# Kernel tuning notes

Measured on AMD Instinct MI355X. Metric: run time of the kernel, lower is better.

The kernel has to match this reference:

```python
import math
import jax, jax.numpy as jnp
from jax import lax
import numpy as np

B, T, DIM = 2, 1024, 512
EXPAND, D_STATE, CONV_K, NUM_SCALES = 2, 16, 4, 3
D_INNER = EXPAND * DIM
DT_RANK = D_INNER // 16


def parallel_scan_log(log_coeffs, log_values):
    # h_t = a_t*h_{t-1} + b_t via Heinsen log-space scan
    a_star = jnp.cumsum(log_coeffs, axis=1)
    return jnp.exp(a_star + lax.cumlogsumexp(log_values - a_star, axis=1))


def selective_scan(x, dt, A, B_ssm, C_ssm, D_p):
    Bb, Tt, di = x.shape
    ds = A.shape[1]
    dt = jax.nn.softplus(dt)
    dA = jnp.exp(dt[..., None] * A[None, None])                    # (B,T,di,ds)
    dBx = dt[..., None] * B_ssm[:, :, None, :] * x[..., None]      # (B,T,di,ds)
    log_dA = jnp.log(jnp.maximum(dA, 1e-38)).reshape(Bb, Tt, di * ds)
    log_dBx = jnp.log(jnp.maximum(dBx, 1e-38)).reshape(Bb, Tt, di * ds)
    h = parallel_scan_log(log_dA, log_dBx).reshape(Bb, Tt, di, ds)
    return jnp.einsum('bts,btds->btd', C_ssm, h) + D_p * x


def ssm_core(x, conv_w, conv_b, xproj_w, dtproj_w, dtproj_b, A_log, D_p):
    di = x.shape[-1]
    # depthwise causal conv1d: left-pad K-1 (== torch pad K-1 both sides + truncate to T)
    xc = lax.conv_general_dilated(x.transpose(0, 2, 1), conv_w, (1,), [(CONV_K - 1, 0)],
                                  dimension_numbers=('NCH', 'OIH', 'NCH'),
                                  feature_group_count=di)
    xc = jax.nn.silu((xc + conv_b[None, :, None]).transpose(0, 2, 1))
    proj = xc @ xproj_w.T
    dt_raw = proj[..., :DT_RANK]
    B_ssm = proj[..., DT_RANK:DT_RANK + D_STATE]
    C_ssm = proj[..., DT_RANK + D_STATE:]
    dt = dt_raw @ dtproj_w.T + dtproj_b
    A = -jnp.exp(A_log)
    return selective_scan(xc, dt, A, B_ssm, C_ssm, D_p)


def downsample(x, stride):
    if stride == 1:
        return x
    Bb, Tt, Dd = x.shape
    Tt2 = Tt // stride * stride
    return x[:, :Tt2].reshape(Bb, Tt2 // stride, stride, Dd).mean(axis=2)


def upsample(x, T_target):
    Bb, T_src, Dd = x.shape
    if T_src == T_target:
        return x
    factor = math.ceil(T_target / T_src)
    x_up = jnp.repeat(x, factor, axis=1)[:, :T_target]
    if x_up.shape[1] < T_target:
        pad = jnp.broadcast_to(x_up[:, -1:], (Bb, T_target - x_up.shape[1], Dd))
        x_up = jnp.concatenate([x_up, pad], axis=1)
    return x_up


def forward(x, in_proj_w, conv_w, conv_b, xproj_w, dtproj_w, dtproj_b, A_log, D_p,
            scale_weights, cg_w1, cg_w2, out_proj_w, ln_gamma, ln_beta):
    Tt = x.shape[1]
    residual = x
    xz = x @ in_proj_w.T
    x_in, gate = xz[..., :D_INNER], xz[..., D_INNER:]
    outs = []
    for s in range(NUM_SCALES):
        x_s = downsample(x_in, 2 ** s)
        y_s = ssm_core(x_s, conv_w[s], conv_b[s], xproj_w[s], dtproj_w[s],
                       dtproj_b[s], A_log[s], D_p[s])
        outs.append(upsample(y_s, Tt))
    w = jax.nn.softmax(scale_weights)
    fused = sum(w[s] * outs[s] for s in range(NUM_SCALES))
    ctx = jnp.mean(jnp.stack(outs, axis=0), axis=0)
    cg = jax.nn.sigmoid(jax.nn.silu(ctx @ cg_w1.T) @ cg_w2.T)
    fused = fused * cg
    out = (fused * jax.nn.silu(gate)) @ out_proj_w.T
    y = out + residual
    mu = jnp.mean(y, axis=-1, keepdims=True)
    var = jnp.var(y, axis=-1, keepdims=True)
    return (y - mu) / jnp.sqrt(var + 1e-5) * ln_gamma + ln_beta


def setup_inputs():
    key = jax.random.key(0)
    ks = jax.random.split(key, 12)
    x = jax.random.normal(ks[0], (B, T, DIM), jnp.float32)
    in_proj_w = jax.random.normal(ks[1], (2 * D_INNER, DIM), jnp.float32) * (1.0 / math.sqrt(DIM))
    conv_w = jax.random.normal(ks[2], (NUM_SCALES, D_INNER, 1, CONV_K), jnp.float32) * 0.3
    conv_b = jax.random.normal(ks[3], (NUM_SCALES, D_INNER), jnp.float32) * 0.05
    xproj_w = jax.random.normal(ks[4], (NUM_SCALES, DT_RANK + 2 * D_STATE, D_INNER), jnp.float32) * 0.02
    dtproj_w = jax.random.normal(ks[5], (NUM_SCALES, D_INNER, DT_RANK), jnp.float32) * 0.05
    dtproj_b = jax.random.uniform(ks[6], (NUM_SCALES, D_INNER), jnp.float32,
                                  math.log(0.001), math.log(0.1))
    A_log = jnp.broadcast_to(jnp.log(jnp.arange(1, D_STATE + 1, dtype=jnp.float32)),
                             (NUM_SCALES, D_INNER, D_STATE))
    D_p = jnp.ones((NUM_SCALES, D_INNER), jnp.float32)
    scale_weights = jnp.ones((NUM_SCALES,), jnp.float32)
    cg_w1 = jax.random.normal(ks[7], (D_INNER // 2, D_INNER), jnp.float32) * (1.0 / math.sqrt(D_INNER))
    cg_w2 = jax.random.normal(ks[8], (D_INNER, D_INNER // 2), jnp.float32) * (1.0 / math.sqrt(D_INNER // 2))
    out_proj_w = jax.random.normal(ks[9], (DIM, D_INNER), jnp.float32) * (1.0 / math.sqrt(D_INNER))
    ln_gamma = jnp.ones((DIM,), jnp.float32)
    ln_beta = jnp.zeros((DIM,), jnp.float32)
    return {"x": x, "in_proj_w": in_proj_w, "conv_w": conv_w, "conv_b": conv_b,
            "xproj_w": xproj_w, "dtproj_w": dtproj_w, "dtproj_b": dtproj_b,
            "A_log": A_log, "D_p": D_p, "scale_weights": scale_weights,
            "cg_w1": cg_w1, "cg_w2": cg_w2, "out_proj_w": out_proj_w,
            "ln_gamma": ln_gamma, "ln_beta": ln_beta}


def reference(x, in_proj_w, conv_w, conv_b, xproj_w, dtproj_w, dtproj_b, A_log, D_p,
              scale_weights, cg_w1, cg_w2, out_proj_w, ln_gamma, ln_beta):
    return forward(x, in_proj_w, conv_w, conv_b, xproj_w, dtproj_w, dtproj_b, A_log,
                   D_p, scale_weights, cg_w1, cg_w2, out_proj_w, ln_gamma, ln_beta)
```

## Files before the change

### kernel.cpp

```cpp
#include <hip/hip_runtime.h>
#include <hip/hip_bf16.h>

#define BATCH   2
#define SEQ     1024
#define DIMSZ   512
#define DINNER  1024
#define DTRANK  64
#define DSTATE  16
#define CHUNK   32

typedef __hip_bfloat16 bf16;
typedef __attribute__((ext_vector_type(8))) short s8v;
typedef __attribute__((ext_vector_type(4))) float f4v;

constexpr size_t OXH    = 0;
constexpr size_t OXL    = 1048576;
constexpr size_t OIPWH  = 2097152;
constexpr size_t OIPWL  = 3145728;
constexpr size_t OXWH   = 4194304;
constexpr size_t OXWL   = 4489216;
constexpr size_t ODTWH  = 4784128;
constexpr size_t ODTWL  = 4980736;
constexpr size_t OCG1H  = 5177344;
constexpr size_t OCG1L  = 5701632;
constexpr size_t OCG2H  = 6225920;
constexpr size_t OCG2L  = 6750208;
constexpr size_t OOPWH  = 7274496;
constexpr size_t OOPWL  = 7798784;
constexpr size_t OPJDTH = 8323072;
constexpr size_t OPJDTL = 8552448;
constexpr size_t OH1H   = 8781824;
constexpr size_t OH1L   = 9830400;
constexpr size_t OFGH   = 10878976;
constexpr size_t OFGL   = 12976128;

__device__ __forceinline__ float sigmoidf_(float x) { return 1.f / (1.f + __expf(-x)); }
__device__ __forceinline__ float siluf_(float x) { return x * sigmoidf_(x); }
__device__ __forceinline__ void split2(float v, bf16& hi, bf16& lo) {
    hi = __float2bfloat16(v);
    lo = __float2bfloat16(v - __bfloat162float(hi));
}
__device__ __forceinline__ void split_store4(const float4 v,
                                             bf16* __restrict__ ph,
                                             bf16* __restrict__ pl) {
    union { bf16 b[4]; uint2 u; } H, L;
    split2(v.x, H.b[0], L.b[0]); split2(v.y, H.b[1], L.b[1]);
    split2(v.z, H.b[2], L.b[2]); split2(v.w, H.b[3], L.b[3]);
    *reinterpret_cast<uint2*>(ph) = H.u;
    *reinterpret_cast<uint2*>(pl) = L.u;
}

__global__ void split_inputs_kernel(
    const float* __restrict__ x,   const float* __restrict__ ipw,
    const float* __restrict__ xw,  const float* __restrict__ dtw,
    const float* __restrict__ c1,  const float* __restrict__ c2,
    const float* __restrict__ opw, bf16* __restrict__ bws)
{
    int blk = blockIdx.x;
    const float* src; size_t off, sz;
    if (blk < 1024)      { src = x;   off = OXH;   sz = 1048576; }
    else if (blk < 2048) { src = ipw; off = OIPWH; sz = 1048576; blk -= 1024; }
    else if (blk < 2336) { src = xw;  off = OXWH;  sz = 294912;  blk -= 2048; }
    else if (blk < 2528) { src = dtw; off = ODTWH; sz = 196608;  blk -= 2336; }
    else if (blk < 3040) { src = c1;  off = OCG1H; sz = 524288;  blk -= 2528; }
    else if (blk < 3552) { src = c2;  off = OCG2H; sz = 524288;  blk -= 3040; }
    else                 { src = opw; off = OOPWH; sz = 524288;  blk -= 3552; }
    int i = blk * 1024 + threadIdx.x * 4;
    float4 v = *reinterpret_cast<const float4*>(src + i);
    split_store4(v, bws + off + i, bws + off + sz + i);
}

template <int ACT, bool ADD_RES, bool DT_MODE, bool CTX_A, bool GATE3, bool OUT_SPLIT>
__global__ __launch_bounds__(256) void mgemm_kernel(
    const bf16* __restrict__ Agh, const bf16* __restrict__ Agl, int lda, int K,
    const bf16* __restrict__ Bgh, const bf16* __restrict__ Bgl,
    const float* __restrict__ bias,
    const float* __restrict__ res,
    const float* __restrict__ gxz,
    const float* __restrict__ yy0,
    const float* __restrict__ yy1,
    const float* __restrict__ yy2,
    const float* __restrict__ swp,
    float* __restrict__ C, bf16* __restrict__ Ch, bf16* __restrict__ Cl, int N)
{
    __shared__ bf16 Ah[64][72], Al[64][72], Bh[64][72], Bl[64][72];

    const int m0 = blockIdx.x * 64;
    const int n0 = blockIdx.y * 64;
    const int tid = threadIdx.x;
    const int wave = tid >> 6;
    const int lane = tid & 63;
    const int wm = (wave >> 1) * 32;
    const int wn = (wave & 1) * 32;
    const int m16 = lane & 15;
    const int q   = lane >> 4;

    int scale = 0;
    if (DT_MODE) scale = (m0 < 2048) ? 0 : ((m0 < 3072) ? 1 : 2);
    const bf16* Bhp = DT_MODE ? (Bgh + (size_t)scale * 1024 * K) : Bgh;
    const bf16* Blp = DT_MODE ? (Bgl + (size_t)scale * 1024 * K) : Bgl;
    const float* bias_p = (ACT == 3) ? (DT_MODE ? bias + (size_t)scale * N : bias) : nullptr;

    f4v acc[2][2];
#pragma unroll
    for (int i = 0; i < 2; i++)
#pragma unroll
        for (int j = 0; j < 2; j++)
#pragma unroll
            for (int r = 0; r < 4; r++) acc[i][j][r] = 0.f;

    const int cch = tid & 15;
    const int c4  = cch * 4;
    const int r0  = tid >> 4;

    const float* a0p[4]; const float* a1p[4]; const float* a2p[4];
    const bf16*  ahp[4]; const bf16*  alp[4];
#pragma unroll
    for (int p = 0; p < 4; p++) {
        int m = m0 + r0 + p * 16;
        if (CTX_A) {
            int b = m >> 10, t = m & 1023;
            a0p[p] = yy0 + (size_t)m * 1024 + c4;
            a1p[p] = yy1 + (size_t)((b << 9) + (t >> 1)) * 1024 + c4;
            a2p[p] = yy2 + (size_t)((b << 8) + (t >> 2)) * 1024 + c4;
        } else {
            ahp[p] = Agh + (size_t)m * lda + c4;
            alp[p] = Agl + (size_t)m * lda + c4;
        }
    }
    const bf16* Bh_b = Bhp + (size_t)(n0 + r0) * K + c4;
    const bf16* Bl_b = Blp + (size_t)(n0 + r0) * K + c4;

    const int nkt = K >> 6;
    float4 raf[4]; uint2 rah[4], ral[4], rbh[4], rbl[4];
#pragma unroll
    for (int p = 0; p < 4; p++) {
        if (CTX_A) {
            float4 u = *reinterpret_cast<const float4*>(a0p[p]);
            float4 v = *reinterpret_cast<const float4*>(a1p[p]);
            float4 w = *reinterpret_cast<const float4*>(a2p[p]);
            raf[p] = make_float4((u.x + v.x + w.x) * (1.f / 3.f), (u.y + v.y + w.y) * (1.f / 3.f),
                                 (u.z + v.z + w.z) * (1.f / 3.f), (u.w + v.w + w.w) * (1.f / 3.f));
        } else {
            rah[p] = *reinterpret_cast<const uint2*>(ahp[p]);
            ral[p] = *reinterpret_cast<const uint2*>(alp[p]);
        }
        rbh[p] = *reinterpret_cast<const uint2*>(Bh_b + (size_t)(p * 16) * K);
        rbl[p] = *reinterpret_cast<const uint2*>(Bl_b + (size_t)(p * 16) * K);
    }

    for (int kt = 0; kt < nkt; kt++) {
        if (kt) __syncthreads();
#pragma unroll
        for (int p = 0; p < 4; p++) {
            int r = r0 + p * 16;
            if (CTX_A) {
                split_store4(raf[p], &Ah[r][c4], &Al[r][c4]);
            } else {
                *reinterpret_cast<uint2*>(&Ah[r][c4]) = rah[p];
                *reinterpret_cast<uint2*>(&Al[r][c4]) = ral[p];
            }
            *reinterpret_cast<uint2*>(&Bh[r][c4]) = rbh[p];
            *reinterpret_cast<uint2*>(&Bl[r][c4]) = rbl[p];
        }
        __syncthreads();
        if (kt + 1 < nkt) {
            int off = (kt + 1) * 64;
#pragma unroll
            for (int p = 0; p < 4; p++) {
                if (CTX_A) {
                    float4 u = *reinterpret_cast<const float4*>(a0p[p] + off);
                    float4 v = *reinterpret_cast<const float4*>(a1p[p] + off);
                    float4 w = *reinterpret_cast<const float4*>(a2p[p] + off);
                    raf[p] = make_float4((u.x + v.x + w.x) * (1.f / 3.f), (u.y + v.y + w.y) * (1.f / 3.f),
                                         (u.z + v.z + w.z) * (1.f / 3.f), (u.w + v.w + w.w) * (1.f / 3.f));
                } else {
                    rah[p] = *reinterpret_cast<const uint2*>(ahp[p] + off);
                    ral[p] = *reinterpret_cast<const uint2*>(alp[p] + off);
                }
                rbh[p] = *reinterpret_cast<const uint2*>(Bh_b + off + (size_t)(p * 16) * K);
                rbl[p] = *reinterpret_cast<const uint2*>(Bl_b + off + (size_t)(p * 16) * K);
            }
        }
#pragma unroll
        for (int kk = 0; kk < 2; kk++) {
            const int col = kk * 32 + q * 8;
            s8v ah[2], al[2], bh[2], bl[2];
#pragma unroll
            for (int i = 0; i < 2; i++) {
                int ar = wm + i * 16 + m16;
                ah[i] = *reinterpret_cast<const s8v*>(&Ah[ar][col]);
                al[i] = *reinterpret_cast<const s8v*>(&Al[ar][col]);
                int br = wn + i * 16 + m16;
                bh[i] = *reinterpret_cast<const s8v*>(&Bh[br][col]);
                bl[i] = *reinterpret_cast<const s8v*>(&Bl[br][col]);
            }
#pragma unroll
            for (int i = 0; i < 2; i++)
#pragma unroll
                for (int j = 0; j < 2; j++) {
                    acc[i][j] = __builtin_amdgcn_mfma_f32_16x16x32_bf16(ah[i], bh[j], acc[i][j], 0, 0, 0);
                    acc[i][j] = __builtin_amdgcn_mfma_f32_16x16x32_bf16(al[i], bh[j], acc[i][j], 0, 0, 0);
                    acc[i][j] = __builtin_amdgcn_mfma_f32_16x16x32_bf16(ah[i], bl[j], acc[i][j], 0, 0, 0);
                }
        }
    }

    float e0 = 0.f, e1 = 0.f, e2 = 0.f, inv = 0.f;
    if (GATE3) {
        float s0 = swp[0], s1 = swp[1], s2 = swp[2];
        float mx = fmaxf(s0, fmaxf(s1, s2));
        e0 = __expf(s0 - mx); e1 = __expf(s1 - mx); e2 = __expf(s2 - mx);
        inv = 1.f / (e0 + e1 + e2);
    }

#pragma unroll
    for (int i = 0; i < 2; i++) {
#pragma unroll
        for (int j = 0; j < 2; j++) {
#pragma unroll
            for (int r = 0; r < 4; r++) {
                int gm = m0 + wm + i * 16 + q * 4 + r;
                int gn = n0 + wn + j * 16 + m16;
                float v = acc[i][j][r];
                if (ACT == 3) { v += bias_p[gn]; v = (v > 20.f) ? v : __logf(1.f + __expf(v)); }
                else if (ACT == 1) v = siluf_(v);
                else if (ACT == 2) v = sigmoidf_(v);
                if (GATE3) {
                    int b = gm >> 10, t = gm & 1023;
                    float f = (e0 * yy0[(size_t)gm * 1024 + gn]
                             + e1 * yy1[(size_t)((b << 9) + (t >> 1)) * 1024 + gn]
                             + e2 * yy2[(size_t)((b << 8) + (t >> 2)) * 1024 + gn]) * inv;
                    v = f * v * siluf_(gxz[(size_t)gm * 2048 + 1024 + gn]);
                } else if (ADD_RES) {
                    v += res[(size_t)gm * N + gn];
                }
                if (OUT_SPLIT) {
                    bf16 hh, ll; split2(v, hh, ll);
                    Ch[(size_t)gm * N + gn] = hh;
                    Cl[(size_t)gm * N + gn] = ll;
                } else {
                    C[(size_t)gm * N + gn] = v;
                }
            }
        }
    }
}

__global__ __launch_bounds__(256) void xproj_mfma_kernel(
    const float* __restrict__ A,
    const bf16* __restrict__ xwh, const bf16* __restrict__ xwl,
    float* __restrict__ pj, bf16* __restrict__ pjdth, bf16* __restrict__ pjdtl)
{
    const int K = 1024;
    __shared__ bf16 Ah[64][72], Al[64][72], Bh[64][72], Bl[64][72];

    const int m0 = blockIdx.x * 64;
    const int n0 = blockIdx.y * 64;
    const int tid = threadIdx.x;
    const int wave = tid >> 6;
    const int lane = tid & 63;
    const int wm = (wave >> 1) * 32;
    const int wn = (wave & 1) * 32;
    const int m16 = lane & 15;
    const int q   = lane >> 4;

    const int scale = (m0 < 2048) ? 0 : ((m0 < 3072) ? 1 : 2);
    const bf16* Bhp = xwh + (size_t)scale * 96 * K;
    const bf16* Blp = xwl + (size_t)scale * 96 * K;

    f4v acc[2][2];
#pragma unroll
    for (int i = 0; i < 2; i++)
#pragma unroll
        for (int j = 0; j < 2; j++)
#pragma unroll
            for (int r = 0; r < 4; r++) acc[i][j][r] = 0.f;

    const int cch = tid & 15;
    const int c4  = cch * 4;
    const int r0  = tid >> 4;

    const float* Abase = A + (size_t)(m0 + r0) * K + c4;
    const bf16* Bh_b = Bhp + (size_t)(n0 + r0) * K + c4;
    const bf16* Bl_b = Blp + (size_t)(n0 + r0) * K + c4;
    bool bok[4];
#pragma unroll
    for (int p = 0; p < 4; p++) bok[p] = (n0 + r0 + p * 16) < 96;

    const int nkt = K >> 6;
    float4 ra[4]; uint2 rbh[4], rbl[4];
    const uint2 zero2 = make_uint2(0u, 0u);
#pragma unroll
    for (int p = 0; p < 4; p++) {
        ra[p] = *reinterpret_cast<const float4*>(Abase + (size_t)(p * 16) * K);
        rbh[p] = bok[p] ? *reinterpret_cast<const uint2*>(Bh_b + (size_t)(p * 16) * K) : zero2;
        rbl[p] = bok[p] ? *reinterpret_cast<const uint2*>(Bl_b + (size_t)(p * 16) * K) : zero2;
    }

    for (int kt = 0; kt < nkt; kt++) {
        if (kt) __syncthreads();
#pragma unroll
        for (int p = 0; p < 4; p++) {
            int r = r0 + p * 16;
            split_store4(ra[p], &Ah[r][c4], &Al[r][c4]);
            *reinterpret_cast<uint2*>(&Bh[r][c4]) = rbh[p];
            *reinterpret_cast<uint2*>(&Bl[r][c4]) = rbl[p];
        }
        __syncthreads();
        if (kt + 1 < nkt) {
            int off = (kt + 1) * 64;
#pragma unroll
            for (int p = 0; p < 4; p++) {
                ra[p] = *reinterpret_cast<const float4*>(Abase + off + (size_t)(p * 16) * K);
                rbh[p] = bok[p] ? *reinterpret_cast<const uint2*>(Bh_b + off + (size_t)(p * 16) * K) : zero2;
                rbl[p] = bok[p] ? *reinterpret_cast<const uint2*>(Bl_b + off + (size_t)(p * 16) * K) : zero2;
            }
        }
#pragma unroll
        for (int kk = 0; kk < 2; kk++) {
            const int col = kk * 32 + q * 8;
            s8v ah[2], al[2], bh[2], bl[2];
#pragma unroll
            for (int i = 0; i < 2; i++) {
                int ar = wm + i * 16 + m16;
                ah[i] = *reinterpret_cast<const s8v*>(&Ah[ar][col]);
                al[i] = *reinterpret_cast<const s8v*>(&Al[ar][col]);
                int br = wn + i * 16 + m16;
                bh[i] = *reinterpret_cast<const s8v*>(&Bh[br][col]);
                bl[i] = *reinterpret_cast<const s8v*>(&Bl[br][col]);
            }
#pragma unroll
            for (int i = 0; i < 2; i++)
#pragma unroll
                for (int j = 0; j < 2; j++) {
                    acc[i][j] = __builtin_amdgcn_mfma_f32_16x16x32_bf16(ah[i], bh[j], acc[i][j], 0, 0, 0);
                    acc[i][j] = __builtin_amdgcn_mfma_f32_16x16x32_bf16(al[i], bh[j], acc[i][j], 0, 0, 0);
                    acc[i][j] = __builtin_amdgcn_mfma_f32_16x16x32_bf16(ah[i], bl[j], acc[i][j], 0, 0, 0);
                }
        }
    }

#pragma unroll
    for (int i = 0; i < 2; i++) {
#pragma unroll
        for (int j = 0; j < 2; j++) {
            int gn = n0 + wn + j * 16 + m16;
            if (gn >= 96) continue;
#pragma unroll
            for (int r = 0; r < 4; r++) {
                int gm = m0 + wm + i * 16 + q * 4 + r;
                float v = acc[i][j][r];
                pj[(size_t)gm * 96 + gn] = v;
                if (gn < 64) {
                    bf16 hh, ll; split2(v, hh, ll);
                    pjdth[(size_t)gm * 64 + gn] = hh;
                    pjdtl[(size_t)gm * 64 + gn] = ll;
                }
            }
        }
    }
}

__global__ void conv_fused_kernel(const float* __restrict__ xz,
                                  const float* __restrict__ cw,
                                  const float* __restrict__ cb,
                                  float* __restrict__ xc)
{
    int idx = blockIdx.x * blockDim.x + threadIdx.x;
    if (idx >= 3670016) return;
    int s, rel;
    if (idx < 2097152)      { s = 0; rel = idx; }
    else if (idx < 3145728) { s = 1; rel = idx - 2097152; }
    else                    { s = 2; rel = idx - 3145728; }
    int c = rel & 1023;
    int row = rel >> 10;
    int Ts = 1024 >> s;
    int b = row / Ts;
    int t = row - b * Ts;
    const float* base = xz + (size_t)(b * 1024) * 2048 + c;

    float acc = cb[s * 1024 + c];
#pragma unroll
    for (int k = 0; k < 4; k++) {
        int tau = t - 3 + k;
        if (tau < 0) continue;
        float xv;
        if (s == 0) {
            xv = base[(size_t)tau * 2048];
        } else if (s == 1) {
            xv = 0.5f * (base[(size_t)(2 * tau) * 2048] + base[(size_t)(2 * tau + 1) * 2048]);
        } else {
            xv = 0.25f * (base[(size_t)(4 * tau) * 2048] + base[(size_t)(4 * tau + 1) * 2048]
                        + base[(size_t)(4 * tau + 2) * 2048] + base[(size_t)(4 * tau + 3) * 2048]);
        }
        acc = fmaf(cw[(s * 1024 + c) * 4 + k], xv, acc);
    }
    xc[idx] = siluf_(acc);
}

__device__ __forceinline__ void scan_decode(int blk, int& s, int& nchunk, int& Ts,
                                            int& dquad, int& chunk, int& b, size_t& soff)
{
    int local;
    if (blk < 256)      { s = 0; local = blk;       soff = 0; }
    else if (blk < 384) { s = 1; local = blk - 256; soff = 1048576; }
    else                { s = 2; local = blk - 384; soff = 1572864; }
    nchunk = 32 >> s;
    Ts = 1024 >> s;
    dquad = local & 3;
    chunk = (local >> 2) & (nchunk - 1);
    b = local >> (7 - s);
}

__global__ __launch_bounds__(256) void scan_pass1(
    const float* __restrict__ dt0, const float* __restrict__ xc0, const float* __restrict__ pj0,
    const float* __restrict__ dt1, const float* __restrict__ xc1, const float* __restrict__ pj1,
    const float* __restrict__ dt2, const float* __restrict__ xc2, const float* __restrict__ pj2,
    const float* __restrict__ A_log,
    float* __restrict__ prodA_buf, float* __restrict__ h_buf)
{
    const int jhalf = (blockIdx.x >= 448) ? 1 : 0;
    const int jo = jhalf * 8;
    int s, nchunk, Ts, dquad, chunk, b; size_t soff;
    scan_decode(blockIdx.x - jhalf * 448, s, nchunk, Ts, dquad, chunk, b, soff);
    const float* dt = (s == 0) ? dt0 : (s == 1) ? dt1 : dt2;
    const float* xc = (s == 0) ? xc0 : (s == 1) ? xc1 : xc2;
    const float* pj = (s == 0) ? pj0 : (s == 1) ? pj1 : pj2;

    const int d = dquad * 256 + threadIdx.x;
    const size_t rowbase = (size_t)b * Ts;
    const int t0 = chunk * CHUNK;

    float Acoef[8], h[8], p[8];
#pragma unroll
    for (int j = 0; j < 8; j++) {
        Acoef[j] = -__expf(A_log[((size_t)(s * DINNER + d)) * 16 + jo + j]);
        h[j] = 0.f; p[j] = 1.f;
    }

    __shared__ float bcB[CHUNK][8];
    if (threadIdx.x < CHUNK * 8) {
        int i = threadIdx.x >> 3, jj = threadIdx.x & 7;
        bcB[i][jj] = pj[(rowbase + t0 + i) * 96 + 64 + jo + jj];
    }
    __syncthreads();

    for (int i = 0; i < CHUNK; i++) {
        size_t t = rowbase + t0 + i;
        float dtv = dt[t * DINNER + d];
        float xv  = xc[t * DINNER + d];
#pragma unroll
        for (int j = 0; j < 8; j++) {
            float dA  = fmaxf(__expf(dtv * Acoef[j]), 1e-38f);
            float dbx = fmaxf(dtv * bcB[i][j] * xv, 1e-38f);
            h[j] = fmaf(dA, h[j], dbx);
            p[j] *= dA;
        }
    }

    size_t base = soff + (size_t)((b * nchunk + chunk) * 16 + jo) * 1024 + d;
#pragma unroll
    for (int j = 0; j < 8; j++) {
        prodA_buf[base + (size_t)j * 1024] = p[j];
        h_buf[base + (size_t)j * 1024] = h[j];
    }
}

__global__ __launch_bounds__(256) void scan_pass2(
    const float* __restrict__ dt0, const float* __restrict__ xc0,
    const float* __restrict__ pj0,
    const float* __restrict__ dt1, const float* __restrict__ xc1,
    const float* __restrict__ pj1,
    const float* __restrict__ dt2, const float* __restrict__ xc2,
    const float* __restrict__ pj2,
    float* __restrict__ ya0, float* __restrict__ ya1, float* __restrict__ ya2,
    float* __restrict__ yb0, float* __restrict__ yb1, float* __restrict__ yb2,
    const float* __restrict__ A_log, const float* __restrict__ D_p,
    const float* __restrict__ prodA_buf, const float* __restrict__ h_buf)
{
    const int jhalf = (blockIdx.x >= 448) ? 1 : 0;
    const int jo = jhalf * 8;
    int s, nchunk, Ts, dquad, chunk, b; size_t soff;
    scan_decode(blockIdx.x - jhalf * 448, s, nchunk, Ts, dquad, chunk, b, soff);
    const float* dt = (s == 0) ? dt0 : (s == 1) ? dt1 : dt2;
    const float* xc = (s == 0) ? xc0 : (s == 1) ? xc1 : xc2;
    const float* pj = (s == 0) ? pj0 : (s == 1) ? pj1 : pj2;
    float* y = jhalf ? ((s == 0) ? yb0 : (s == 1) ? yb1 : yb2)
                     : ((s == 0) ? ya0 : (s == 1) ? ya1 : ya2);

    const int d = dquad * 256 + threadIdx.x;
    const size_t rowbase = (size_t)b * Ts;
    const int t0 = chunk * CHUNK;

    float Acoef[8], h[8];
#pragma unroll
    for (int j = 0; j < 8; j++) {
        Acoef[j] = -__expf(A_log[((size_t)(s * DINNER + d)) * 16 + jo + j]);
        h[j] = 0.f;
    }
    const float Dp = (jhalf == 0) ? D_p[s * DINNER + d] : 0.f;

    for (int c = 0; c < chunk; c++) {
        size_t cb = soff + (size_t)((b * nchunk + c) * 16 + jo) * 1024 + d;
#pragma unroll
        for (int j = 0; j < 8; j++)
            h[j] = fmaf(prodA_buf[cb + (size_t)j * 1024], h[j], h_buf[cb + (size_t)j * 1024]);
    }

    __shared__ float bc[CHUNK][16];
    for (int u = threadIdx.x; u < CHUNK * 16; u += 256) {
        int i = u >> 4, jj = u & 15;
        int col = (jj < 8) ? (64 + jo + jj) : (80 + jo + (jj - 8));
        bc[i][jj] = pj[(rowbase + t0 + i) * 96 + col];
    }
    __syncthreads();

    for (int i = 0; i < CHUNK; i++) {
        size_t t = rowbase + t0 + i;
        float dtv = dt[t * DINNER + d];
        float xv  = xc[t * DINNER + d];
        float accy = 0.f;
#pragma unroll
        for (int j = 0; j < 8; j++) {
            float dA  = fmaxf(__expf(dtv * Acoef[j]), 1e-38f);
            float dbx = fmaxf(dtv * bc[i][j] * xv, 1e-38f);
            h[j] = fmaf(dA, h[j], dbx);
            accy = fmaf(bc[i][8 + j], h[j], accy);
        }
        y[t * DINNER + d] = accy + Dp * xv;
    }
}

__global__ void combine_y_kernel(const float* __restrict__ ya,
                                 const float* __restrict__ yb,
                                 float* __restrict__ ysum)
{
    int idx = blockIdx.x * blockDim.x + threadIdx.x;
    float4 a = reinterpret_cast<const float4*>(ya)[idx];
    float4 b = reinterpret_cast<const float4*>(yb)[idx];
    reinterpret_cast<float4*>(ysum)[idx] =
        make_float4(a.x + b.x, a.y + b.y, a.z + b.z, a.w + b.w);
}

__global__ __launch_bounds__(256) void ln_kernel(
    const float* __restrict__ yin, const float* __restrict__ gamma,
    const float* __restrict__ beta, float* __restrict__ out)
{
    int token = blockIdx.x;
    int tid = threadIdx.x;
    const float* row = yin + (size_t)token * DIMSZ;
    float v0 = row[tid], v1 = row[tid + 256];
    __shared__ float s1[256], s2[256];
    s1[tid] = v0 + v1;
    s2[tid] = v0 * v0 + v1 * v1;
    __syncthreads();
    for (int off = 128; off > 0; off >>= 1) {
        if (tid < off) { s1[tid] += s1[tid + off]; s2[tid] += s2[tid + off]; }
        __syncthreads();
    }
    float mu = s1[0] * (1.f / 512.f);
    float var = s2[0] * (1.f / 512.f) - mu * mu;
    float rstd = rsqrtf(var + 1e-5f);
    float* orow = out + (size_t)token * DIMSZ;
    orow[tid]       = (v0 - mu) * rstd * gamma[tid]       + beta[tid];
    orow[tid + 256] = (v1 - mu) * rstd * gamma[tid + 256] + beta[tid + 256];
}

extern "C" void kernel_launch(void* const* d_in, const int* in_sizes, int n_in,
                              void* d_out, int out_size, void* d_ws, size_t ws_size,
                              hipStream_t stream)
{
    const float* x         = (const float*)d_in[0];
    const float* in_proj_w = (const float*)d_in[1];
    const float* conv_w    = (const float*)d_in[2];
    const float* conv_b    = (const float*)d_in[3];
    const float* xproj_w   = (const float*)d_in[4];
    const float* dtproj_w  = (const float*)d_in[5];
    const float* dtproj_b  = (const float*)d_in[6];
    const float* A_log     = (const float*)d_in[7];
    const float* D_p       = (const float*)d_in[8];
    const float* scale_w   = (const float*)d_in[9];
    const float* cg_w1     = (const float*)d_in[10];
    const float* cg_w2     = (const float*)d_in[11];
    const float* out_pw    = (const float*)d_in[12];
    const float* ln_gamma  = (const float*)d_in[13];
    const float* ln_beta   = (const float*)d_in[14];
    float* out = (float*)d_out;

    float* ws = (float*)d_ws;
    float* xz    = ws;
    float* xc0   = xz    + 4194304;
    float* xc1   = xc0   + 2097152;
    float* xc2   = xc1   + 1048576;
    float* pj0   = xc2   + 524288;
    float* pj1   = pj0   + 196608;
    float* pj2   = pj1   + 98304;
    float* dt0   = pj2   + 49152;
    float* dt1   = dt0   + 2097152;
    float* dt2   = dt1   + 1048576;
    float* ya0   = dt2   + 524288;
    float* ya1   = ya0   + 2097152;
    float* ya2   = ya1   + 1048576;
    float* yb0   = ya2   + 524288;
    float* yb1   = yb0   + 2097152;
    float* yb2   = yb1   + 1048576;
    float* prodA = yb2   + 524288;
    float* hbuf  = prodA + 1835008;

    bf16* bws = (bf16*)(ws + 23887872);
    const bf16 *xh   = bws + OXH,   *xl   = bws + OXL;
    const bf16 *ipwh = bws + OIPWH, *ipwl = bws + OIPWL;
    const bf16 *xwh  = bws + OXWH,  *xwl  = bws + OXWL;
    const bf16 *dtwh = bws + ODTWH, *dtwl = bws + ODTWL;
    const bf16 *cg1h = bws + OCG1H, *cg1l = bws + OCG1L;
    const bf16 *cg2h = bws + OCG2H, *cg2l = bws + OCG2L;
    const bf16 *opwh = bws + OOPWH, *opwl = bws + OOPWL;
    bf16 *pjdth = bws + OPJDTH, *pjdtl = bws + OPJDTL;
    bf16 *h1h   = bws + OH1H,   *h1l   = bws + OH1L;
    bf16 *fgh   = bws + OFGH,   *fgl   = bws + OFGL;

    float* ysum0  = dt0;
    float* ysum1  = dt0 + 2097152;
    float* ysum2  = dt0 + 3145728;
    float* outpre = prodA;

    split_inputs_kernel<<<4064, 256, 0, stream>>>(
        x, in_proj_w, xproj_w, dtproj_w, cg_w1, cg_w2, out_pw, bws);

    mgemm_kernel<0, false, false, false, false, false><<<dim3(32, 32), 256, 0, stream>>>(
        xh, xl, DIMSZ, DIMSZ, ipwh, ipwl, nullptr, nullptr, nullptr,
        nullptr, nullptr, nullptr, nullptr, xz, nullptr, nullptr, 2048);

    conv_fused_kernel<<<14336, 256, 0, stream>>>(xz, conv_w, conv_b, xc0);

    xproj_mfma_kernel<<<dim3(56, 2), 256, 0, stream>>>(xc0, xwh, xwl, pj0, pjdth, pjdtl);

    mgemm_kernel<3, false, true, false, false, false><<<dim3(56, 16), 256, 0, stream>>>(
        pjdth, pjdtl, DTRANK, DTRANK, dtwh, dtwl, dtproj_b, nullptr, nullptr,
        nullptr, nullptr, nullptr, nullptr, dt0, nullptr, nullptr, 1024);

    scan_pass1<<<896, 256, 0, stream>>>(dt0, xc0, pj0, dt1, xc1, pj1,
                                        dt2, xc2, pj2, A_log, prodA, hbuf);
    scan_pass2<<<896, 256, 0, stream>>>(dt0, xc0, pj0, dt1, xc1, pj1,
                                        dt2, xc2, pj2,
                                        ya0, ya1, ya2, yb0, yb1, yb2,
                                        A_log, D_p, prodA, hbuf);

    combine_y_kernel<<<3584, 256, 0, stream>>>(ya0, yb0, ysum0);

    mgemm_kernel<1, false, false, true, false, true><<<dim3(32, 8), 256, 0, stream>>>(
        nullptr, nullptr, DINNER, DINNER, cg1h, cg1l, nullptr, nullptr, nullptr,
        ysum0, ysum1, ysum2, nullptr, nullptr, h1h, h1l, 512);

    mgemm_kernel<2, false, false, false, true, true><<<dim3(32, 16), 256, 0, stream>>>(
        h1h, h1l, DIMSZ, DIMSZ, cg2h, cg2l, nullptr, nullptr, xz,
        ysum0, ysum1, ysum2, scale_w, nullptr, fgh, fgl, 1024);

    mgemm_kernel<0, true, false, false, false, false><<<dim3(32, 8), 256, 0, stream>>>(
        fgh, fgl, DINNER, DINNER, opwh, opwl, nullptr, x, nullptr,
        nullptr, nullptr, nullptr, nullptr, outpre, nullptr, nullptr, 512);

    ln_kernel<<<BATCH * SEQ, 256, 0, stream>>>(outpre, ln_gamma, ln_beta, out);
}
```

Measured before the change: 292.8 us.

## Interleave bf16 hi/lo split operands and add chunk-carry prefix kernel for scan

Stores the hi and lo bf16 halves of each 4-element group side by side, so GEMM operand loads become single 16-byte loads instead of two 8-byte loads from separate arrays. The scan's second pass no longer has every chunk serially recompute its carry from all earlier chunks. A new prefix kernel computes the per-chunk carries once, and pass2 then handles all 16 states per thread, which removes the split y buffers and the combine kernel. The cost is an extra kernel launch, half as many pass2 blocks, and more registers per thread in pass2.

```diff
diff --git a/kernel.cpp b/kernel.cpp
--- a/kernel.cpp
+++ b/kernel.cpp
@@ -13,32 +13,28 @@
 typedef __attribute__((ext_vector_type(8))) short s8v;
 typedef __attribute__((ext_vector_type(4))) float f4v;
 
-constexpr size_t OXH    = 0;
-constexpr size_t OXL    = 1048576;
-constexpr size_t OIPWH  = 2097152;
-constexpr size_t OIPWL  = 3145728;
-constexpr size_t OXWH   = 4194304;
-constexpr size_t OXWL   = 4489216;
-constexpr size_t ODTWH  = 4784128;
-constexpr size_t ODTWL  = 4980736;
-constexpr size_t OCG1H  = 5177344;
-constexpr size_t OCG1L  = 5701632;
-constexpr size_t OCG2H  = 6225920;
-constexpr size_t OCG2L  = 6750208;
-constexpr size_t OOPWH  = 7274496;
-constexpr size_t OOPWL  = 7798784;
-constexpr size_t OPJDTH = 8323072;
-constexpr size_t OPJDTL = 8552448;
-constexpr size_t OH1H   = 8781824;
-constexpr size_t OH1L   = 9830400;
-constexpr size_t OFGH   = 10878976;
-constexpr size_t OFGL   = 12976128;
+constexpr size_t OXI   = 0;
+constexpr size_t OIPI  = 2097152;
+constexpr size_t OXWI  = 4194304;
+constexpr size_t ODTI  = 4784128;
+constexpr size_t OC1I  = 5177344;
+constexpr size_t OC2I  = 6225920;
+constexpr size_t OOPI  = 7274496;
+constexpr size_t OPJI  = 8323072;
+constexpr size_t OH1I  = 8781824;
+constexpr size_t OFGI  = 10878976;
 
 __device__ __forceinline__ float sigmoidf_(float x) { return 1.f / (1.f + __expf(-x)); }
 __device__ __forceinline__ float siluf_(float x) { return x * sigmoidf_(x); }
 __device__ __forceinline__ void split2(float v, bf16& hi, bf16& lo) {
     hi = __float2bfloat16(v);
     lo = __float2bfloat16(v - __bfloat162float(hi));
+}
+__device__ __forceinline__ void split_store4i(const float4 v, bf16* __restrict__ p) {
+    union { bf16 b[8]; uint4 q; } U;
+    split2(v.x, U.b[0], U.b[4]); split2(v.y, U.b[1], U.b[5]);
+    split2(v.z, U.b[2], U.b[6]); split2(v.w, U.b[3], U.b[7]);
+    *reinterpret_cast<uint4*>(p) = U.q;
 }
 __device__ __forceinline__ void split_store4(const float4 v,
                                              bf16* __restrict__ ph,
@@ -57,23 +53,23 @@
     const float* __restrict__ opw, bf16* __restrict__ bws)
 {
     int blk = blockIdx.x;
-    const float* src; size_t off, sz;
-    if (blk < 1024)      { src = x;   off = OXH;   sz = 1048576; }
-    else if (blk < 2048) { src = ipw; off = OIPWH; sz = 1048576; blk -= 1024; }
-    else if (blk < 2336) { src = xw;  off = OXWH;  sz = 294912;  blk -= 2048; }
-    else if (blk < 2528) { src = dtw; off = ODTWH; sz = 196608;  blk -= 2336; }
-    else if (blk < 3040) { src = c1;  off = OCG1H; sz = 524288;  blk -= 2528; }
-    else if (blk < 3552) { src = c2;  off = OCG2H; sz = 524288;  blk -= 3040; }
-    else                 { src = opw; off = OOPWH; sz = 524288;  blk -= 3552; }
+    const float* src; size_t off;
+    if (blk < 1024)      { src = x;   off = OXI;  }
+    else if (blk < 2048) { src = ipw; off = OIPI; blk -= 1024; }
+    else if (blk < 2336) { src = xw;  off = OXWI; blk -= 2048; }
+    else if (blk < 2528) { src = dtw; off = ODTI; blk -= 2336; }
+    else if (blk < 3040) { src = c1;  off = OC1I; blk -= 2528; }
+    else if (blk < 3552) { src = c2;  off = OC2I; blk -= 3040; }
+    else                 { src = opw; off = OOPI; blk -= 3552; }
     int i = blk * 1024 + threadIdx.x * 4;
     float4 v = *reinterpret_cast<const float4*>(src + i);
-    split_store4(v, bws + off + i, bws + off + sz + i);
+    split_store4i(v, bws + off + (size_t)i * 2);
 }
 
 template <int ACT, bool ADD_RES, bool DT_MODE, bool CTX_A, bool GATE3, bool OUT_SPLIT>
 __global__ __launch_bounds__(256) void mgemm_kernel(
-    const bf16* __restrict__ Agh, const bf16* __restrict__ Agl, int lda, int K,
-    const bf16* __restrict__ Bgh, const bf16* __restrict__ Bgl,
+    const bf16* __restrict__ Ai, int lda, int K,
+    const bf16* __restrict__ Bi,
     const float* __restrict__ bias,
     const float* __restrict__ res,
     const float* __restrict__ gxz,
@@ -81,7 +77,7 @@
     const float* __restrict__ yy1,
     const float* __restrict__ yy2,
     const float* __restrict__ swp,
-    float* __restrict__ C, bf16* __restrict__ Ch, bf16* __restrict__ Cl, int N)
+    float* __restrict__ C, bf16* __restrict__ Ci, int N)
 {
     __shared__ bf16 Ah[64][72], Al[64][72], Bh[64][72], Bl[64][72];
 
@@ -97,8 +93,7 @@
 
     int scale = 0;
     if (DT_MODE) scale = (m0 < 2048) ? 0 : ((m0 < 3072) ? 1 : 2);
-    const bf16* Bhp = DT_MODE ? (Bgh + (size_t)scale * 1024 * K) : Bgh;
-    const bf16* Blp = DT_MODE ? (Bgl + (size_t)scale * 1024 * K) : Bgl;
+    const bf16* Bip = DT_MODE ? (Bi + (size_t)scale * 1024 * K * 2) : Bi;
     const float* bias_p = (ACT == 3) ? (DT_MODE ? bias + (size_t)scale * N : bias) : nullptr;
 
     f4v acc[2][2];
@@ -114,7 +109,7 @@
     const int r0  = tid >> 4;
 
     const float* a0p[4]; const float* a1p[4]; const float* a2p[4];
-    const bf16*  ahp[4]; const bf16*  alp[4];
+    const bf16*  aip[4];
 #pragma unroll
     for (int p = 0; p < 4; p++) {
         int m = m0 + r0 + p * 16;
@@ -124,12 +119,10 @@
             a1p[p] = yy1 + (size_t)((b << 9) + (t >> 1)) * 1024 + c4;
             a2p[p] = yy2 + (size_t)((b << 8) + (t >> 2)) * 1024 + c4;
         } else {
-            ahp[p] = Agh + (size_t)m * lda + c4;
-            alp[p] = Agl + (size_t)m * lda + c4;
-        }
-    }
-    const bf16* Bh_b = Bhp + (size_t)(n0 + r0) * K + c4;
-    const bf16* Bl_b = Blp + (size_t)(n0 + r0) * K + c4;
+            aip[p] = Ai + ((size_t)m * lda + c4) * 2;
+        }
+    }
+    const bf16* Bi_b = Bip + ((size_t)(n0 + r0) * K + c4) * 2;
 
     const int nkt = K >> 6;
     float4 raf[4]; uint2 rah[4], ral[4], rbh[4], rbl[4];
@@ -142,11 +135,11 @@
             raf[p] = make_float4((u.x + v.x + w.x) * (1.f / 3.f), (u.y + v.y + w.y) * (1.f / 3.f),
                                  (u.z + v.z + w.z) * (1.f / 3.f), (u.w + v.w + w.w) * (1.f / 3.f));
         } else {
-            rah[p] = *reinterpret_cast<const uint2*>(ahp[p]);
-            ral[p] = *reinterpret_cast<const uint2*>(alp[p]);
-        }
-        rbh[p] = *reinterpret_cast<const uint2*>(Bh_b + (size_t)(p * 16) * K);
-        rbl[p] = *reinterpret_cast<const uint2*>(Bl_b + (size_t)(p * 16) * K);
+            uint4 ua = *reinterpret_cast<const uint4*>(aip[p]);
+            rah[p] = make_uint2(ua.x, ua.y); ral[p] = make_uint2(ua.z, ua.w);
+        }
+        uint4 ub = *reinterpret_cast<const uint4*>(Bi_b + (size_t)(p * 16) * K * 2);
+        rbh[p] = make_uint2(ub.x, ub.y); rbl[p] = make_uint2(ub.z, ub.w);
     }
 
     for (int kt = 0; kt < nkt; kt++) {
@@ -175,11 +168,11 @@
                     raf[p] = make_float4((u.x + v.x + w.x) * (1.f / 3.f), (u.y + v.y + w.y) * (1.f / 3.f),
                                          (u.z + v.z + w.z) * (1.f / 3.f), (u.w + v.w + w.w) * (1.f / 3.f));
                 } else {
-                    rah[p] = *reinterpret_cast<const uint2*>(ahp[p] + off);
-                    ral[p] = *reinterpret_cast<const uint2*>(alp[p] + off);
+                    uint4 ua = *reinterpret_cast<const uint4*>(aip[p] + (size_t)off * 2);
+                    rah[p] = make_uint2(ua.x, ua.y); ral[p] = make_uint2(ua.z, ua.w);
                 }
-                rbh[p] = *reinterpret_cast<const uint2*>(Bh_b + off + (size_t)(p * 16) * K);
-                rbl[p] = *reinterpret_cast<const uint2*>(Bl_b + off + (size_t)(p * 16) * K);
+                uint4 ub = *reinterpret_cast<const uint4*>(Bi_b + ((size_t)(p * 16) * K + off) * 2);
+                rbh[p] = make_uint2(ub.x, ub.y); rbl[p] = make_uint2(ub.z, ub.w);
             }
         }
 #pragma unroll
@@ -237,8 +230,9 @@
                 }
                 if (OUT_SPLIT) {
                     bf16 hh, ll; split2(v, hh, ll);
-                    Ch[(size_t)gm * N + gn] = hh;
-                    Cl[(size_t)gm * N + gn] = ll;
+                    size_t gb = ((size_t)gm * N + (gn & ~3)) * 2 + (gn & 3);
+                    Ci[gb] = hh;
+                    Ci[gb + 4] = ll;
                 } else {
                     C[(size_t)gm * N + gn] = v;
                 }
@@ -249,8 +243,8 @@
 
 __global__ __launch_bounds__(256) void xproj_mfma_kernel(
     const float* __restrict__ A,
-    const bf16* __restrict__ xwh, const bf16* __restrict__ xwl,
-    float* __restrict__ pj, bf16* __restrict__ pjdth, bf16* __restrict__ pjdtl)
+    const bf16* __restrict__ xwi,
+    float* __restrict__ pj, bf16* __restrict__ pjdti)
 {
     const int K = 1024;
     __shared__ bf16 Ah[64][72], Al[64][72], Bh[64][72], Bl[64][72];
@@ -266,8 +260,7 @@
     const int q   = lane >> 4;
 
     const int scale = (m0 < 2048) ? 0 : ((m0 < 3072) ? 1 : 2);
-    const bf16* Bhp = xwh + (size_t)scale * 96 * K;
-    const bf16* Blp = xwl + (size_t)scale * 96 * K;
+    const bf16* Bip = xwi + (size_t)scale * 96 * K * 2;
 
     f4v acc[2][2];
 #pragma unroll
@@ -282,20 +275,20 @@
     const int r0  = tid >> 4;
 
     const float* Abase = A + (size_t)(m0 + r0) * K + c4;
-    const bf16* Bh_b = Bhp + (size_t)(n0 + r0) * K + c4;
-    const bf16* Bl_b = Blp + (size_t)(n0 + r0) * K + c4;
+    const bf16* Bi_b = Bip + ((size_t)(n0 + r0) * K + c4) * 2;
     bool bok[4];
 #pragma unroll
     for (int p = 0; p < 4; p++) bok[p] = (n0 + r0 + p * 16) < 96;
 
     const int nkt = K >> 6;
     float4 ra[4]; uint2 rbh[4], rbl[4];
-    const uint2 zero2 = make_uint2(0u, 0u);
 #pragma unroll
     for (int p = 0; p < 4; p++) {
         ra[p] = *reinterpret_cast<const float4*>(Abase + (size_t)(p * 16) * K);
-        rbh[p] = bok[p] ? *reinterpret_cast<const uint2*>(Bh_b + (size_t)(p * 16) * K) : zero2;
-        rbl[p] = bok[p] ? *reinterpret_cast<const uint2*>(Bl_b + (size_t)(p * 16) * K) : zero2;
+        if (bok[p]) {
+            uint4 ub = *reinterpret_cast<const uint4*>(Bi_b + (size_t)(p * 16) * K * 2);
+            rbh[p] = make_uint2(ub.x, ub.y); rbl[p] = make_uint2(ub.z, ub.w);
+        } else { rbh[p] = make_uint2(0u, 0u); rbl[p] = make_uint2(0u, 0u); }
     }
 
     for (int kt = 0; kt < nkt; kt++) {
@@ -313,8 +306,10 @@
 #pragma unroll
             for (int p = 0; p < 4; p++) {
                 ra[p] = *reinterpret_cast<const float4*>(Abase + off + (size_t)(p * 16) * K);
-                rbh[p] = bok[p] ? *reinterpret_cast<const uint2*>(Bh_b + off + (size_t)(p * 16) * K) : zero2;
-                rbl[p] = bok[p] ? *reinterpret_cast<const uint2*>(Bl_b + off + (size_t)(p * 16) * K) : zero2;
+                if (bok[p]) {
+                    uint4 ub = *reinterpret_cast<const uint4*>(Bi_b + ((size_t)(p * 16) * K + off) * 2);
+                    rbh[p] = make_uint2(ub.x, ub.y); rbl[p] = make_uint2(ub.z, ub.w);
+                }
             }
         }
 #pragma unroll
@@ -354,8 +349,9 @@
                 pj[(size_t)gm * 96 + gn] = v;
                 if (gn < 64) {
                     bf16 hh, ll; split2(v, hh, ll);
-                    pjdth[(size_t)gm * 64 + gn] = hh;
-                    pjdtl[(size_t)gm * 64 + gn] = ll;
+                    size_t gb = ((size_t)gm * 64 + (gn & ~3)) * 2 + (gn & 3);
+                    pjdti[gb] = hh;
+                    pjdti[gb + 4] = ll;
                 }
             }
         }
@@ -467,6 +463,30 @@
     }
 }
 
+__global__ __launch_bounds__(256) void scan_prefix_kernel(
+    const float* __restrict__ prodA_buf, float* __restrict__ h_buf)
+{
+    int blk = blockIdx.x;
+    int s; size_t soff;
+    if (blk < 128)      { s = 0; soff = 0; }
+    else if (blk < 256) { s = 1; soff = 1048576; blk -= 128; }
+    else                { s = 2; soff = 1572864; blk -= 256; }
+    const int nchunk = 32 >> s;
+    const int b  = blk >> 6;
+    const int j  = (blk >> 2) & 15;
+    const int dq = blk & 3;
+    const int d  = dq * 256 + threadIdx.x;
+
+    float H = 0.f;
+    for (int c = 0; c < nchunk; c++) {
+        size_t idx = soff + (size_t)((b * nchunk + c) * 16 + j) * 1024 + d;
+        float p = prodA_buf[idx];
+        float h = h_buf[idx];
+        h_buf[idx] = H;
+        H = fmaf(p, H, h);
+    }
+}
+
 __global__ __launch_bounds__(256) void scan_pass2(
     const float* __restrict__ dt0, const float* __restrict__ xc0,
     const float* __restrict__ pj0,
@@ -474,45 +494,34 @@
     const float* __restrict__ pj1,
     const float* __restrict__ dt2, const float* __restrict__ xc2,
     const float* __restrict__ pj2,
-    float* __restrict__ ya0, float* __restrict__ ya1, float* __restrict__ ya2,
-    float* __restrict__ yb0, float* __restrict__ yb1, float* __restrict__ yb2,
+    float* __restrict__ y0, float* __restrict__ y1, float* __restrict__ y2,
     const float* __restrict__ A_log, const float* __restrict__ D_p,
-    const float* __restrict__ prodA_buf, const float* __restrict__ h_buf)
-{
-    const int jhalf = (blockIdx.x >= 448) ? 1 : 0;
-    const int jo = jhalf * 8;
+    const float* __restrict__ carry)
+{
     int s, nchunk, Ts, dquad, chunk, b; size_t soff;
-    scan_decode(blockIdx.x - jhalf * 448, s, nchunk, Ts, dquad, chunk, b, soff);
+    scan_decode(blockIdx.x, s, nchunk, Ts, dquad, chunk, b, soff);
     const float* dt = (s == 0) ? dt0 : (s == 1) ? dt1 : dt2;
     const float* xc = (s == 0) ? xc0 : (s == 1) ? xc1 : xc2;
     const float* pj = (s == 0) ? pj0 : (s == 1) ? pj1 : pj2;
-    float* y = jhalf ? ((s == 0) ? yb0 : (s == 1) ? yb1 : yb2)
-                     : ((s == 0) ? ya0 : (s == 1) ? ya1 : ya2);
+    float* y = (s == 0) ? y0 : (s == 1) ? y1 : y2;
 
     const int d = dquad * 256 + threadIdx.x;
     const size_t rowbase = (size_t)b * Ts;
     const int t0 = chunk * CHUNK;
 
-    float Acoef[8], h[8];
-#pragma unroll
-    for (int j = 0; j < 8; j++) {
-        Acoef[j] = -__expf(A_log[((size_t)(s * DINNER + d)) * 16 + jo + j]);
-        h[j] = 0.f;
-    }
-    const float Dp = (jhalf == 0) ? D_p[s * DINNER + d] : 0.f;
-
-    for (int c = 0; c < chunk; c++) {
-        size_t cb = soff + (size_t)((b * nchunk + c) * 16 + jo) * 1024 + d;
-#pragma unroll
-        for (int j = 0; j < 8; j++)
-            h[j] = fmaf(prodA_buf[cb + (size_t)j * 1024], h[j], h_buf[cb + (size_t)j * 1024]);
-    }
-
-    __shared__ float bc[CHUNK][16];
-    for (int u = threadIdx.x; u < CHUNK * 16; u += 256) {
-        int i = u >> 4, jj = u & 15;
-        int col = (jj < 8) ? (64 + jo + jj) : (80 + jo + (jj - 8));
-        bc[i][jj] = pj[(rowbase + t0 + i) * 96 + col];
+    float Acoef[16], h[16];
+    const size_t cb = soff + (size_t)((b * nchunk + chunk) * 16) * 1024 + d;
+#pragma unroll
+    for (int j = 0; j < 16; j++) {
+        Acoef[j] = -__expf(A_log[((size_t)(s * DINNER + d)) * 16 + j]);
+        h[j] = carry[cb + (size_t)j * 1024];
+    }
+    const float Dp = D_p[s * DINNER + d];
+
+    __shared__ float bc[CHUNK][32];
+    for (int u = threadIdx.x; u < CHUNK * 32; u += 256) {
+        int i = u >> 5, jj = u & 31;
+        bc[i][jj] = pj[(rowbase + t0 + i) * 96 + 64 + jj];
     }
     __syncthreads();
 
@@ -522,25 +531,14 @@
         float xv  = xc[t * DINNER + d];
         float accy = 0.f;
 #pragma unroll
-        for (int j = 0; j < 8; j++) {
+        for (int j = 0; j < 16; j++) {
             float dA  = fmaxf(__expf(dtv * Acoef[j]), 1e-38f);
             float dbx = fmaxf(dtv * bc[i][j] * xv, 1e-38f);
             h[j] = fmaf(dA, h[j], dbx);
-            accy = fmaf(bc[i][8 + j], h[j], accy);
+            accy = fmaf(bc[i][16 + j], h[j], accy);
         }
         y[t * DINNER + d] = accy + Dp * xv;
     }
-}
-
-__global__ void combine_y_kernel(const float* __restrict__ ya,
-                                 const float* __restrict__ yb,
-                                 float* __restrict__ ysum)
-{
-    int idx = blockIdx.x * blockDim.x + threadIdx.x;
-    float4 a = reinterpret_cast<const float4*>(ya)[idx];
-    float4 b = reinterpret_cast<const float4*>(yb)[idx];
-    reinterpret_cast<float4*>(ysum)[idx] =
-        make_float4(a.x + b.x, a.y + b.y, a.z + b.z, a.w + b.w);
 }
 
 __global__ __launch_bounds__(256) void ln_kernel(
@@ -599,67 +597,59 @@
     float* dt0   = pj2   + 49152;
     float* dt1   = dt0   + 2097152;
     float* dt2   = dt1   + 1048576;
-    float* ya0   = dt2   + 524288;
-    float* ya1   = ya0   + 2097152;
-    float* ya2   = ya1   + 1048576;
-    float* yb0   = ya2   + 524288;
-    float* yb1   = yb0   + 2097152;
-    float* yb2   = yb1   + 1048576;
-    float* prodA = yb2   + 524288;
+    float* y0    = dt2   + 524288;
+    float* y1    = y0    + 2097152;
+    float* y2    = y1    + 1048576;
+    float* prodA = y2    + 524288 + 3670016;
     float* hbuf  = prodA + 1835008;
 
     bf16* bws = (bf16*)(ws + 23887872);
-    const bf16 *xh   = bws + OXH,   *xl   = bws + OXL;
-    const bf16 *ipwh = bws + OIPWH, *ipwl = bws + OIPWL;
-    const bf16 *xwh  = bws + OXWH,  *xwl  = bws + OXWL;
-    const bf16 *dtwh = bws + ODTWH, *dtwl = bws + ODTWL;
-    const bf16 *cg1h = bws + OCG1H, *cg1l = bws + OCG1L;
-    const bf16 *cg2h = bws + OCG2H, *cg2l = bws + OCG2L;
-    const bf16 *opwh = bws + OOPWH, *opwl = bws + OOPWL;
-    bf16 *pjdth = bws + OPJDTH, *pjdtl = bws + OPJDTL;
-    bf16 *h1h   = bws + OH1H,   *h1l   = bws + OH1L;
-    bf16 *fgh   = bws + OFGH,   *fgl   = bws + OFGL;
-
-    float* ysum0  = dt0;
-    float* ysum1  = dt0 + 2097152;
-    float* ysum2  = dt0 + 3145728;
+    const bf16 *xi   = bws + OXI;
+    const bf16 *ipwi = bws + OIPI;
+    const bf16 *xwi  = bws + OXWI;
+    const bf16 *dtwi = bws + ODTI;
+    const bf16 *c1i  = bws + OC1I;
+    const bf16 *c2i  = bws + OC2I;
+    const bf16 *opwi = bws + OOPI;
+    bf16 *pjdti = bws + OPJI;
+    bf16 *h1i   = bws + OH1I;
+    bf16 *fgi   = bws + OFGI;
+
     float* outpre = prodA;
 
     split_inputs_kernel<<<4064, 256, 0, stream>>>(
         x, in_proj_w, xproj_w, dtproj_w, cg_w1, cg_w2, out_pw, bws);
 
     mgemm_kernel<0, false, false, false, false, false><<<dim3(32, 32), 256, 0, stream>>>(
-        xh, xl, DIMSZ, DIMSZ, ipwh, ipwl, nullptr, nullptr, nullptr,
-        nullptr, nullptr, nullptr, nullptr, xz, nullptr, nullptr, 2048);
+        xi, DIMSZ, DIMSZ, ipwi, nullptr, nullptr, nullptr,
+        nullptr, nullptr, nullptr, nullptr, xz, nullptr, 2048);
 
     conv_fused_kernel<<<14336, 256, 0, stream>>>(xz, conv_w, conv_b, xc0);
 
-    xproj_mfma_kernel<<<dim3(56, 2), 256, 0, stream>>>(xc0, xwh, xwl, pj0, pjdth, pjdtl);
+    xproj_mfma_kernel<<<dim3(56, 2), 256, 0, stream>>>(xc0, xwi, pj0, pjdti);
 
     mgemm_kernel<3, false, true, false, false, false><<<dim3(56, 16), 256, 0, stream>>>(
-        pjdth, pjdtl, DTRANK, DTRANK, dtwh, dtwl, dtproj_b, nullptr, nullptr,
-        nullptr, nullptr, nullptr, nullptr, dt0, nullptr, nullptr, 1024);
+        pjdti, DTRANK, DTRANK, dtwi, dtproj_b, nullptr, nullptr,
+        nullptr, nullptr, nullptr, nullptr, dt0, nullptr, 1024);
 
     scan_pass1<<<896, 256, 0, stream>>>(dt0, xc0, pj0, dt1, xc1, pj1,
                                         dt2, xc2, pj2, A_log, prodA, hbuf);
-    scan_pass2<<<896, 256, 0, stream>>>(dt0, xc0, pj0, dt1, xc1, pj1,
+    scan_prefix_kernel<<<384, 256, 0, stream>>>(prodA, hbuf);
+    scan_pass2<<<448, 256, 0, stream>>>(dt0, xc0, pj0, dt1, xc1, pj1,
                                         dt2, xc2, pj2,
-                                        ya0, ya1, ya2, yb0, yb1, yb2,
-                                        A_log, D_p, prodA, hbuf);
-
-    combine_y_kernel<<<3584, 256, 0, stream>>>(ya0, yb0, ysum0);
+                                        y0, y1, y2, A_log, D_p, hbuf);
 
     mgemm_kernel<1, false, false, true, false, true><<<dim3(32, 8), 256, 0, stream>>>(
-        nullptr, nullptr, DINNER, DINNER, cg1h, cg1l, nullptr, nullptr, nullptr,
-        ysum0, ysum1, ysum2, nullptr, nullptr, h1h, h1l, 512);
+        nullptr, DINNER, DINNER, c1i, nullptr, nullptr, nullptr,
+        y0, y1, y2, nullptr, nullptr, h1i, 512);
 
     mgemm_kernel<2, false, false, false, true, true><<<dim3(32, 16), 256, 0, stream>>>(
-        h1h, h1l, DIMSZ, DIMSZ, cg2h, cg2l, nullptr, nullptr, xz,
-        ysum0, ysum1, ysum2, scale_w, nullptr, fgh, fgl, 1024);
+        h1i, DIMSZ, DIMSZ, c2i, nullptr, nullptr, xz,
+        y0, y1, y2, scale_w, nullptr, fgi, 1024);
 
     mgemm_kernel<0, true, false, false, false, false><<<dim3(32, 8), 256, 0, stream>>>(
-        fgh, fgl, DINNER, DINNER, opwh, opwl, nullptr, x, nullptr,
-        nullptr, nullptr, nullptr, nullptr, outpre, nullptr, nullptr, 512);
+        fgi, DINNER, DINNER, opwi, nullptr, x, nullptr,
+        nullptr, nullptr, nullptr, nullptr, outpre, nullptr, 512);
 
     ln_kernel<<<BATCH * SEQ, 256, 0, stream>>>(outpre, ln_gamma, ln_beta, out);
 }
```

After: 284.5 us. -2.8%, faster.
